# Kernel tuning notes

Measured on AMD Instinct MI355X. Metric: run time of the kernel, lower is better.

Reference implementation:

```python
import jax, jax.numpy as jnp
import numpy as np

B, S, H, E, TOPK = 8, 512, 1024, 8, 2


def setup_inputs() -> dict:
    key = jax.random.key(0)
    ks = jax.random.split(key, 10)
    D = 2 * H
    inp = {
        "vector": jax.random.normal(ks[0], (B, S, D), dtype=jnp.float32),
        # gate weights (Linear(H, E)): stored as [H, E] for x @ W + b
        "Wg": jax.random.normal(ks[1], (H, E), dtype=jnp.float32) * 0.02,
        "bg": jnp.zeros((E,), dtype=jnp.float32),
        "Wf": jax.random.normal(ks[2], (H, E), dtype=jnp.float32) * 0.02,
        "bf": jnp.zeros((E,), dtype=jnp.float32),
        # expert MLP weights, stacked over experts: Linear(2H,2H) -> ReLU -> Linear(2H,2H)
        "W1": jax.random.normal(ks[3], (E, D, D), dtype=jnp.float32) * 0.02,
        "b1": jnp.zeros((E, D), dtype=jnp.float32),
        "W2": jax.random.normal(ks[4], (E, D, D), dtype=jnp.float32) * 0.02,
        "b2": jnp.zeros((E, D), dtype=jnp.float32),
        # combine weights (config['initializer_weight'])
        "weight": jnp.ones((2,), dtype=jnp.float32),
        "top_k": TOPK,
    }
    return inp


def reference(vector, Wg, bg, Wf, bf, W1, b1, W2, b2, weight, top_k):
    h = Wg.shape[0]
    n_exp = Wg.shape[1]
    # gate_g on first half, softmax, then top-k sparsify (scatter of topk values)
    rout_g = jax.nn.softmax(vector[:, :, :h] @ Wg + bg, axis=-1)           # [B,S,E]
    vals, idx = jax.lax.top_k(rout_g, top_k)                               # [B,S,k]
    route_g = jnp.sum(jax.nn.one_hot(idx, n_exp, dtype=vals.dtype) * vals[..., None], axis=-2)  # [B,S,E]
    # gate_f on second half: dense softmax routing
    rout_f = jax.nn.softmax(vector[:, :, h:2 * h] @ Wf + bf, axis=-1)      # [B,S,E]
    # dense expert computation for every token (dropout = identity at eval)
    hidden = jax.nn.relu(jnp.einsum('bsd,edh->bseh', vector, W1) + b1)     # [B,S,E,2H]
    expert_out = jnp.einsum('bseh,ehd->bsed', hidden, W2) + b2             # [B,S,E,2H]
    out0 = weight[0] * jnp.einsum('bsed,bse->bsd', expert_out[..., :h], route_g)
    out1 = weight[1] * jnp.einsum('bsed,bse->bsd', expert_out[..., h:2 * h], rout_f)
    return (out0, out1)
```

## Files before the change

### kernel.cpp

```cpp
#include <hip/hip_runtime.h>

#define TOKENS 4096
#define DDIM   2048
#define HDIM   1024
#define NEXP   8
#define GK     2048
#define GN     2048

typedef __bf16 bf16_t;
typedef __bf16 bf16x8 __attribute__((ext_vector_type(8)));
typedef __bf16 bf16x4 __attribute__((ext_vector_type(4)));
typedef float  f32x4  __attribute__((ext_vector_type(4)));

__device__ inline void gld_lds16(const bf16_t* g, bf16_t* l) {
  __builtin_amdgcn_global_load_lds(
      (const __attribute__((address_space(1))) void*)g,
      (__attribute__((address_space(3))) void*)l, 16, 0, 0);
}

__global__ __launch_bounds__(256)
void k_routing(const float* __restrict__ vec,
               const float* __restrict__ Wg, const float* __restrict__ bg,
               const float* __restrict__ Wf, const float* __restrict__ bfv,
               const float* __restrict__ wgt,
               float* __restrict__ c0, float* __restrict__ c1)
{
  const int wave = threadIdx.x >> 6;
  const int lane = threadIdx.x & 63;
  const int m = blockIdx.x * 4 + wave;
  const float* v = vec + (size_t)m * DDIM;

  float ag[NEXP], af[NEXP];
#pragma unroll
  for (int e = 0; e < NEXP; ++e) { ag[e] = 0.f; af[e] = 0.f; }

  for (int i = lane; i < HDIM; i += 64) {
    const float xg = v[i];
    const float xf = v[HDIM + i];
    const float4 wg0 = *(const float4*)(Wg + i * NEXP);
    const float4 wg1 = *(const float4*)(Wg + i * NEXP + 4);
    const float4 wf0 = *(const float4*)(Wf + i * NEXP);
    const float4 wf1 = *(const float4*)(Wf + i * NEXP + 4);
    ag[0] += xg * wg0.x; ag[1] += xg * wg0.y; ag[2] += xg * wg0.z; ag[3] += xg * wg0.w;
    ag[4] += xg * wg1.x; ag[5] += xg * wg1.y; ag[6] += xg * wg1.z; ag[7] += xg * wg1.w;
    af[0] += xf * wf0.x; af[1] += xf * wf0.y; af[2] += xf * wf0.z; af[3] += xf * wf0.w;
    af[4] += xf * wf1.x; af[5] += xf * wf1.y; af[6] += xf * wf1.z; af[7] += xf * wf1.w;
  }
#pragma unroll
  for (int e = 0; e < NEXP; ++e) {
#pragma unroll
    for (int off = 32; off >= 1; off >>= 1) {
      ag[e] += __shfl_xor(ag[e], off, 64);
      af[e] += __shfl_xor(af[e], off, 64);
    }
  }
  if (lane == 0) {
    float g[NEXP], f[NEXP];
    float mg = -1e30f, mf = -1e30f;
#pragma unroll
    for (int e = 0; e < NEXP; ++e) {
      g[e] = ag[e] + bg[e]; mg = fmaxf(mg, g[e]);
      f[e] = af[e] + bfv[e]; mf = fmaxf(mf, f[e]);
    }
    float sg = 0.f, sf = 0.f;
#pragma unroll
    for (int e = 0; e < NEXP; ++e) {
      g[e] = expf(g[e] - mg); sg += g[e];
      f[e] = expf(f[e] - mf); sf += f[e];
    }
    const float rg = 1.f / sg, rf = 1.f / sf;
#pragma unroll
    for (int e = 0; e < NEXP; ++e) { g[e] *= rg; f[e] *= rf; }
    int i1 = 0;
#pragma unroll
    for (int e = 1; e < NEXP; ++e) if (g[e] > g[i1]) i1 = e;
    int i2 = (i1 == 0) ? 1 : 0;
#pragma unroll
    for (int e = 0; e < NEXP; ++e) if (e != i1 && g[e] > g[i2]) i2 = e;
    const float w0 = wgt[0], w1 = wgt[1];
#pragma unroll
    for (int e = 0; e < NEXP; ++e) {
      c0[e * TOKENS + m] = (e == i1 || e == i2) ? w0 * g[e] : 0.f;
      c1[e * TOKENS + m] = w1 * f[e];
    }
  }
}

__global__ __launch_bounds__(256)
void k_cvt(const float* __restrict__ in, bf16_t* __restrict__ out)
{
  const size_t i = ((size_t)blockIdx.x * 256 + threadIdx.x) * 8;
  const float4 a = *(const float4*)(in + i);
  const float4 b = *(const float4*)(in + i + 4);
  bf16x8 o;
  o[0] = (bf16_t)a.x; o[1] = (bf16_t)a.y; o[2] = (bf16_t)a.z; o[3] = (bf16_t)a.w;
  o[4] = (bf16_t)b.x; o[5] = (bf16_t)b.y; o[6] = (bf16_t)b.z; o[7] = (bf16_t)b.w;
  *(bf16x8*)(out + i) = o;
}

#define TP 68
__global__ __launch_bounds__(256)
void k_cvt_wt(const float* __restrict__ W, bf16_t* __restrict__ Wt)
{
  __shared__ __attribute__((aligned(16))) bf16_t tile[64 * TP];
  const size_t eoff = (size_t)blockIdx.z * DDIM * DDIM;
  const float* w = W + eoff;
  bf16_t* wt = Wt + eoff;
  const int k0 = blockIdx.x * 64;
  const int n0 = blockIdx.y * 64;
  const int t = threadIdx.x;
  const int c4 = (t & 15) * 4;
  const int rb = (t >> 4) * 4;
#pragma unroll
  for (int rr = 0; rr < 4; ++rr) {
    const int r = rb + rr;
    const float4 v = *(const float4*)(w + (size_t)(k0 + r) * DDIM + n0 + c4);
    tile[(c4 + 0) * TP + r] = (bf16_t)v.x;
    tile[(c4 + 1) * TP + r] = (bf16_t)v.y;
    tile[(c4 + 2) * TP + r] = (bf16_t)v.z;
    tile[(c4 + 3) * TP + r] = (bf16_t)v.w;
  }
  __syncthreads();
  const int nl = t >> 2;
  const int kq = (t & 3) * 16;
  bf16_t* dst = wt + (size_t)(n0 + nl) * DDIM + k0 + kq;
#pragma unroll
  for (int j2 = 0; j2 < 4; ++j2) {
    bf16x4 u = *(const bf16x4*)(&tile[nl * TP + kq + j2 * 4]);
    *(bf16x4*)(dst + j2 * 4) = u;
  }
}

__global__ __launch_bounds__(256, 2)
void k_gemm_relu(const bf16_t* __restrict__ A, const bf16_t* __restrict__ W1t,
                 const float* __restrict__ b1, bf16_t* __restrict__ Hd)
{
  __shared__ __attribute__((aligned(16))) bf16_t As[128 * 32];
  __shared__ __attribute__((aligned(16))) bf16_t Bs[128 * 32];
  const int e = blockIdx.z;
  const bf16_t* Bt = W1t + (size_t)e * GK * GN;
  const float* bias = b1 + (size_t)e * GN;
  bf16_t* H = Hd + (size_t)e * TOKENS * GN;

  const int t = threadIdx.x;
  const int wave = t >> 6;
  const int lane = t & 63;
  const int m0 = blockIdx.x * 128;
  const int n0 = blockIdx.y * 128;
  const int wm = (wave >> 1) << 6;
  const int wn = (wave & 1) << 6;

  f32x4 acc[4][4] = {};

  const bf16_t* aP0 = A + (size_t)(m0 + (t >> 2)) * GK + (t & 3) * 8;
  const bf16_t* aP1 = aP0 + (size_t)64 * GK;
  const bf16_t* bP0 = Bt + (size_t)(n0 + (t >> 2)) * GK + (t & 3) * 8;
  const bf16_t* bP1 = bP0 + (size_t)64 * GK;
  bf16_t* lA0 = As + wave * 512;
  bf16_t* lA1 = As + 2048 + wave * 512;
  bf16_t* lB0 = Bs + wave * 512;
  bf16_t* lB1 = Bs + 2048 + wave * 512;

  const int fr = lane & 15;
  const int kq = (lane >> 4) * 8;

  for (int k0 = 0; k0 < GK; k0 += 32) {
    gld_lds16(aP0 + k0, lA0);
    gld_lds16(aP1 + k0, lA1);
    gld_lds16(bP0 + k0, lB0);
    gld_lds16(bP1 + k0, lB1);
    __syncthreads();
    bf16x8 afr[4], bfr[4];
#pragma unroll
    for (int i = 0; i < 4; ++i) {
      afr[i] = *(const bf16x8*)(As + (wm + i * 16 + fr) * 32 + kq);
      bfr[i] = *(const bf16x8*)(Bs + (wn + i * 16 + fr) * 32 + kq);
    }
#pragma unroll
    for (int i = 0; i < 4; ++i)
#pragma unroll
      for (int j = 0; j < 4; ++j)
        acc[i][j] = __builtin_amdgcn_mfma_f32_16x16x32_bf16(afr[i], bfr[j], acc[i][j], 0, 0, 0);
    __syncthreads();
  }

  const int col = lane & 15;
  const int rq  = (lane >> 4) * 4;
#pragma unroll
  for (int j = 0; j < 4; ++j) {
    const int gn = n0 + wn + j * 16 + col;
    const float bv = bias[gn];
#pragma unroll
    for (int i = 0; i < 4; ++i) {
      const int gm = m0 + wm + i * 16 + rq;
#pragma unroll
      for (int r = 0; r < 4; ++r) {
        float v = acc[i][j][r] + bv;
        v = v > 0.f ? v : 0.f;
        H[(size_t)(gm + r) * GN + gn] = (bf16_t)v;
      }
    }
  }
}

__global__ __launch_bounds__(256, 2)
void k_gemm2_sum(const bf16_t* __restrict__ Hd, const bf16_t* __restrict__ W2t,
                 const float* __restrict__ b2,
                 const float* __restrict__ c0, const float* __restrict__ c1,
                 float* __restrict__ out0, float* __restrict__ out1)
{
  __shared__ __attribute__((aligned(16))) bf16_t As[128 * 32];
  __shared__ __attribute__((aligned(16))) bf16_t Bs[128 * 32];
  __shared__ float cs[NEXP][128];
  __shared__ float bs[NEXP][128];

  const int t = threadIdx.x;
  const int wave = t >> 6;
  const int lane = t & 63;
  const int m0 = blockIdx.x * 128;
  const int n0 = blockIdx.y * 128;
  const int wm = (wave >> 1) << 6;
  const int wn = (wave & 1) << 6;

  const bool hi = (n0 >= HDIM);
  const float* cc = hi ? c1 : c0;

#pragma unroll
  for (int idx = t; idx < NEXP * 128; idx += 256) {
    const int e = idx >> 7, r = idx & 127;
    cs[e][r] = cc[e * TOKENS + m0 + r];
    bs[e][r] = b2[e * DDIM + n0 + r];
  }

  f32x4 fin[4][4] = {};

  const int fr = lane & 15;
  const int kq = (lane >> 4) * 8;
  const int rowOff = (t >> 2);
  const int kOff = (t & 3) * 8;
  bf16_t* lA0 = As + wave * 512;
  bf16_t* lA1 = As + 2048 + wave * 512;
  bf16_t* lB0 = Bs + wave * 512;
  bf16_t* lB1 = Bs + 2048 + wave * 512;

  for (int e = 0; e < NEXP; ++e) {
    const bf16_t* aP0 = Hd + (size_t)e * TOKENS * GK + (size_t)(m0 + rowOff) * GK + kOff;
    const bf16_t* aP1 = aP0 + (size_t)64 * GK;
    const bf16_t* bP0 = W2t + (size_t)e * GN * GK + (size_t)(n0 + rowOff) * GK + kOff;
    const bf16_t* bP1 = bP0 + (size_t)64 * GK;

    f32x4 acc[4][4] = {};
    for (int k0 = 0; k0 < GK; k0 += 32) {
      gld_lds16(aP0 + k0, lA0);
      gld_lds16(aP1 + k0, lA1);
      gld_lds16(bP0 + k0, lB0);
      gld_lds16(bP1 + k0, lB1);
      __syncthreads();
      bf16x8 afr[4], bfr[4];
#pragma unroll
      for (int i = 0; i < 4; ++i) {
        afr[i] = *(const bf16x8*)(As + (wm + i * 16 + fr) * 32 + kq);
        bfr[i] = *(const bf16x8*)(Bs + (wn + i * 16 + fr) * 32 + kq);
      }
#pragma unroll
      for (int i = 0; i < 4; ++i)
#pragma unroll
        for (int j = 0; j < 4; ++j)
          acc[i][j] = __builtin_amdgcn_mfma_f32_16x16x32_bf16(afr[i], bfr[j], acc[i][j], 0, 0, 0);
      __syncthreads();
    }

    const int colL = wn + (lane & 15);
    const int rqL  = wm + (lane >> 4) * 4;
#pragma unroll
    for (int j = 0; j < 4; ++j) {
      const float bv = bs[e][colL + j * 16];
#pragma unroll
      for (int i = 0; i < 4; ++i) {
#pragma unroll
        for (int r = 0; r < 4; ++r) {
          const float ce = cs[e][rqL + i * 16 + r];
          fin[i][j][r] += ce * (acc[i][j][r] + bv);
        }
      }
    }
  }

  const int col = lane & 15;
  const int rq  = (lane >> 4) * 4;
#pragma unroll
  for (int j = 0; j < 4; ++j) {
    const int gn = n0 + wn + j * 16 + col;
    float* obase = hi ? (out1 + (gn - HDIM)) : (out0 + gn);
#pragma unroll
    for (int i = 0; i < 4; ++i) {
      const int gm = m0 + wm + i * 16 + rq;
#pragma unroll
      for (int r = 0; r < 4; ++r)
        obase[(size_t)(gm + r) * HDIM] = fin[i][j][r];
    }
  }
}

__global__ __launch_bounds__(256, 2)
void k_gemm_out(const bf16_t* __restrict__ A, const bf16_t* __restrict__ Bt,
                const float* __restrict__ bias,
                const float* __restrict__ c0, const float* __restrict__ c1,
                float* __restrict__ out0, float* __restrict__ out1, const int accum)
{
  __shared__ __attribute__((aligned(16))) bf16_t As[128 * 32];
  __shared__ __attribute__((aligned(16))) bf16_t Bs[128 * 32];
  const int t = threadIdx.x;
  const int wave = t >> 6;
  const int lane = t & 63;
  const int m0 = blockIdx.x * 128;
  const int n0 = blockIdx.y * 128;
  const int wm = (wave >> 1) << 6;
  const int wn = (wave & 1) << 6;

  f32x4 acc[4][4] = {};

  const bf16_t* aP0 = A + (size_t)(m0 + (t >> 2)) * GK + (t & 3) * 8;
  const bf16_t* aP1 = aP0 + (size_t)64 * GK;
  const bf16_t* bP0 = Bt + (size_t)(n0 + (t >> 2)) * GK + (t & 3) * 8;
  const bf16_t* bP1 = bP0 + (size_t)64 * GK;
  bf16_t* lA0 = As + wave * 512;
  bf16_t* lA1 = As + 2048 + wave * 512;
  bf16_t* lB0 = Bs + wave * 512;
  bf16_t* lB1 = Bs + 2048 + wave * 512;

  const int fr = lane & 15;
  const int kq = (lane >> 4) * 8;

  for (int k0 = 0; k0 < GK; k0 += 32) {
    gld_lds16(aP0 + k0, lA0);
    gld_lds16(aP1 + k0, lA1);
    gld_lds16(bP0 + k0, lB0);
    gld_lds16(bP1 + k0, lB1);
    __syncthreads();
    bf16x8 afr[4], bfr[4];
#pragma unroll
    for (int i = 0; i < 4; ++i) {
      afr[i] = *(const bf16x8*)(As + (wm + i * 16 + fr) * 32 + kq);
      bfr[i] = *(const bf16x8*)(Bs + (wn + i * 16 + fr) * 32 + kq);
    }
#pragma unroll
    for (int i = 0; i < 4; ++i)
#pragma unroll
      for (int j = 0; j < 4; ++j)
        acc[i][j] = __builtin_amdgcn_mfma_f32_16x16x32_bf16(afr[i], bfr[j], acc[i][j], 0, 0, 0);
    __syncthreads();
  }

  const int col = lane & 15;
  const int rq  = (lane >> 4) * 4;
#pragma unroll
  for (int j = 0; j < 4; ++j) {
    const int gn = n0 + wn + j * 16 + col;
    const float bv = bias[gn];
    const bool lo = gn < HDIM;
    float* obase = lo ? (out0 + gn) : (out1 + (gn - HDIM));
    const float* cc = lo ? c0 : c1;
#pragma unroll
    for (int i = 0; i < 4; ++i) {
      const int gmB = m0 + wm + i * 16 + rq;
#pragma unroll
      for (int r = 0; r < 4; ++r) {
        const int gm = gmB + r;
        float v = (acc[i][j][r] + bv) * cc[gm];
        float* dst = obase + (size_t)gm * HDIM;
        if (accum) v += *dst;
        *dst = v;
      }
    }
  }
}

extern "C" void kernel_launch(void* const* d_in, const int* in_sizes, int n_in,
                              void* d_out, int out_size, void* d_ws, size_t ws_size,
                              hipStream_t stream)
{
  const float* vec = (const float*)d_in[0];
  const float* Wg  = (const float*)d_in[1];
  const float* bg  = (const float*)d_in[2];
  const float* Wf  = (const float*)d_in[3];
  const float* bfv = (const float*)d_in[4];
  const float* W1  = (const float*)d_in[5];
  const float* b1  = (const float*)d_in[6];
  const float* W2  = (const float*)d_in[7];
  const float* b2  = (const float*)d_in[8];
  const float* wgt = (const float*)d_in[9];

  float* out0 = (float*)d_out;
  float* out1 = out0 + (size_t)TOKENS * HDIM;

  char* base = (char*)d_ws;
  const size_t XB = (size_t)TOKENS * DDIM * 2;
  const size_t HB = (size_t)NEXP * TOKENS * DDIM * 2;
  const size_t WT = (size_t)NEXP * DDIM * DDIM * 2;

  bf16_t* Xbf = (bf16_t*)base;
  float*  c0  = (float*)(base + XB);
  float*  c1  = c0 + (size_t)NEXP * TOKENS;
  size_t off = XB + 2 * (size_t)NEXP * TOKENS * 4;

  k_routing<<<dim3(TOKENS / 4), 256, 0, stream>>>(vec, Wg, bg, Wf, bfv, wgt, c0, c1);
  k_cvt<<<dim3((TOKENS * DDIM) / 2048), 256, 0, stream>>>(vec, Xbf);

  if (ws_size >= off + HB + 2 * WT) {
    bf16_t* hidden = (bf16_t*)(base + off);
    bf16_t* W1t    = (bf16_t*)(base + off + HB);
    bf16_t* W2t    = (bf16_t*)(base + off + HB + WT);
    k_cvt_wt<<<dim3(32, 32, NEXP), 256, 0, stream>>>(W1, W1t);
    k_cvt_wt<<<dim3(32, 32, NEXP), 256, 0, stream>>>(W2, W2t);
    k_gemm_relu<<<dim3(32, 16, NEXP), 256, 0, stream>>>(Xbf, W1t, b1, hidden);
    k_gemm2_sum<<<dim3(32, 16), 256, 0, stream>>>(hidden, W2t, b2, c0, c1, out0, out1);
  } else {
    bf16_t* hidden = (bf16_t*)(base + off);
    bf16_t* W1t    = hidden + (size_t)TOKENS * DDIM;
    bf16_t* W2t    = W1t + (size_t)DDIM * DDIM;
    for (int e = 0; e < NEXP; ++e) {
      k_cvt_wt<<<dim3(32, 32, 1), 256, 0, stream>>>(W1 + (size_t)e * DDIM * DDIM, W1t);
      k_cvt_wt<<<dim3(32, 32, 1), 256, 0, stream>>>(W2 + (size_t)e * DDIM * DDIM, W2t);
      k_gemm_relu<<<dim3(32, 16, 1), 256, 0, stream>>>(Xbf, W1t, b1 + (size_t)e * DDIM, hidden);
      k_gemm_out<<<dim3(32, 16), 256, 0, stream>>>(
          hidden, W2t, b2 + (size_t)e * DDIM,
          c0 + (size_t)e * TOKENS, c1 + (size_t)e * TOKENS, out0, out1, e > 0);
    }
  }
}
```

Before: 1.072 ms.

## Rewrite both expert GEMMs with 8-wave 256x128 tiles and 4-stage LDS pipeline

Replaces the 4-wave 128x128 expert GEMM kernels with 512-thread kernels. Each block computes a 256x128 tile, and the two GEMMs run as k_gemm1_8p and k_gemm2_8p. Global-to-LDS loads go through a four-buffer ring issued three stages ahead, so loads overlap the MFMA work. The kernels also use an XOR-swizzled LDS layout, explicit vmcnt/lgkmcnt waits with raw barriers, and s_setprio around the MFMA bursts. In exchange, the LDS footprint per block grows, which may limit resident blocks, and the second GEMM's grid shrinks to 256 blocks.

```diff
diff --git a/kernel.cpp b/kernel.cpp
--- a/kernel.cpp
+++ b/kernel.cpp
@@ -17,6 +17,10 @@
       (const __attribute__((address_space(1))) void*)g,
       (__attribute__((address_space(3))) void*)l, 16, 0, 0);
 }
+
+#define LGKM0() asm volatile("s_waitcnt lgkmcnt(0)" ::: "memory")
+#define VMC(n)  asm volatile("s_waitcnt vmcnt(" #n ")" ::: "memory")
+#define BAR()   __builtin_amdgcn_s_barrier()
 
 __global__ __launch_bounds__(256)
 void k_routing(const float* __restrict__ vec,
@@ -131,6 +135,188 @@
   }
 }
 
+
+#define FRG(base, R, KQ) \
+  (*(const bf16x8*)((base) + ((((R) * 32 + (KQ)) ^ ((((R) >> 3) & 1) << 4)))))
+
+#define MFMA_(d, x, y) (d) = __builtin_amdgcn_mfma_f32_16x16x32_bf16((x), (y), (d), 0, 0, 0)
+
+#define PHASE(U, PA, STA, STB, NP) do { \
+    bf16x8 _a[8], _b0, _b1; \
+    _Pragma("unroll") \
+    for (int _i = 0; _i < 8; ++_i) _a[_i] = FRG(AsF + (U) * 8192, wm + _i * 16 + fr, kq); \
+    _b0 = FRG(BsF + (U) * 4096, wn + fr, kq); \
+    _b1 = FRG(BsF + (U) * 4096, wn + 16 + fr, kq); \
+    if ((PA) < (NP)) { STA(PA, (PA) & 3); STB(PA, (PA) & 3); } \
+    BAR(); LGKM0(); \
+    __builtin_amdgcn_s_setprio(1); \
+    _Pragma("unroll") \
+    for (int _i = 0; _i < 8; ++_i) { MFMA_(acc[_i][0], _a[_i], _b0); MFMA_(acc[_i][1], _a[_i], _b1); } \
+    __builtin_amdgcn_s_setprio(0); \
+  } while (0)
+
+#define TILE(U0, U1, PA, PB, STA, STB, NP) do { \
+    PHASE(U0, PA, STA, STB, NP); \
+    BAR(); \
+    PHASE(U1, PB, STA, STB, NP); \
+    if ((PB) < (NP)) { VMC(3); } else { VMC(0); } \
+    BAR(); \
+  } while (0)
+
+__global__ __launch_bounds__(512, 2)
+void k_gemm1_8p(const bf16_t* __restrict__ A, const bf16_t* __restrict__ W1t,
+                const float* __restrict__ b1, bf16_t* __restrict__ Hd)
+{
+  __shared__ __attribute__((aligned(16))) bf16_t AsF[4 * 8192];
+  __shared__ __attribute__((aligned(16))) bf16_t BsF[4 * 4096];
+  const int e = blockIdx.z;
+  const int t = threadIdx.x;
+  const int wave = t >> 6, lane = t & 63;
+  const int m0 = blockIdx.x * 256, n0 = blockIdx.y * 128;
+  const int wm = (wave >> 2) * 128, wn = (wave & 3) * 32;
+  const int fr = lane & 15, kq = (lane >> 4) * 8;
+
+  const int sRw = wave * 16 + (lane >> 2);
+  const int sC  = ((lane & 3) * 8) ^ (((lane >> 5) & 1) << 4);
+  const bf16_t* aSrc = A + (size_t)(m0 + sRw) * GK + sC;
+  const bf16_t* bSrc = W1t + (size_t)e * GN * GK + (size_t)(n0 + sRw) * GK + sC;
+  bf16_t* aDst = AsF + wave * 512;
+  bf16_t* bDst = BsF + wave * 512;
+
+#define STA1(p, u) do { const bf16_t* _s = aSrc + (size_t)(p) * 32; \
+    gld_lds16(_s, aDst + (u) * 8192); \
+    gld_lds16(_s + (size_t)128 * GK, aDst + (u) * 8192 + 4096); } while (0)
+#define STB1(p, u) gld_lds16(bSrc + (size_t)(p) * 32, bDst + (u) * 4096)
+
+  f32x4 acc[8][2] = {};
+
+  STA1(0, 0); STB1(0, 0);
+  STA1(1, 1); STB1(1, 1);
+  STA1(2, 2); STB1(2, 2);
+  asm volatile("s_waitcnt vmcnt(3)" ::: "memory");
+  BAR();
+
+#pragma unroll 1
+  for (int tt = 0; tt < 32; tt += 2) {
+    TILE(0, 1, 2 * tt + 3, 2 * tt + 4, STA1, STB1, 64);
+    TILE(2, 3, 2 * tt + 5, 2 * tt + 6, STA1, STB1, 64);
+  }
+
+  const float* bias = b1 + (size_t)e * DDIM;
+  bf16_t* Hb = Hd + (size_t)e * TOKENS * DDIM;
+  const int ecol = lane & 15, erow = (lane >> 4) * 4;
+#pragma unroll
+  for (int j = 0; j < 2; ++j) {
+    const int gn = n0 + wn + j * 16 + ecol;
+    const float bv = bias[gn];
+#pragma unroll
+    for (int i = 0; i < 8; ++i) {
+      const int gm = m0 + wm + i * 16 + erow;
+#pragma unroll
+      for (int r = 0; r < 4; ++r) {
+        float v = acc[i][j][r] + bv;
+        v = v > 0.f ? v : 0.f;
+        Hb[(size_t)(gm + r) * DDIM + gn] = (bf16_t)v;
+      }
+    }
+  }
+#undef STA1
+#undef STB1
+}
+
+__global__ __launch_bounds__(512, 2)
+void k_gemm2_8p(const bf16_t* __restrict__ Hd, const bf16_t* __restrict__ W2t,
+                const float* __restrict__ b2,
+                const float* __restrict__ c0, const float* __restrict__ c1,
+                float* __restrict__ out0, float* __restrict__ out1)
+{
+  __shared__ __attribute__((aligned(16))) bf16_t AsF[4 * 8192];
+  __shared__ __attribute__((aligned(16))) bf16_t BsF[4 * 4096];
+  __shared__ float cs[NEXP][256];
+  __shared__ float bsh[NEXP][128];
+
+  const int t = threadIdx.x;
+  const int wave = t >> 6, lane = t & 63;
+  const int m0 = blockIdx.x * 256, n0 = blockIdx.y * 128;
+  const int wm = (wave >> 2) * 128, wn = (wave & 3) * 32;
+  const int fr = lane & 15, kq = (lane >> 4) * 8;
+  const bool hi = (n0 >= HDIM);
+  const float* cc = hi ? c1 : c0;
+
+  for (int idx = t; idx < NEXP * 256; idx += 512) {
+    const int ee = idx >> 8, r = idx & 255;
+    cs[ee][r] = cc[ee * TOKENS + m0 + r];
+  }
+  for (int idx = t; idx < NEXP * 128; idx += 512) {
+    const int ee = idx >> 7, r = idx & 127;
+    bsh[ee][r] = b2[ee * DDIM + n0 + r];
+  }
+
+  const int sRw = wave * 16 + (lane >> 2);
+  const int sC  = ((lane & 3) * 8) ^ (((lane >> 5) & 1) << 4);
+  const bf16_t* aSrc = Hd + (size_t)(m0 + sRw) * GK + sC;
+  const bf16_t* bSrc = W2t + (size_t)(n0 + sRw) * GK + sC;
+  bf16_t* aDst = AsF + wave * 512;
+  bf16_t* bDst = BsF + wave * 512;
+
+#define STA2(p, u) do { \
+    const bf16_t* _s = aSrc + (size_t)((p) >> 6) * ((size_t)TOKENS * GK) + (size_t)(((p) & 63) * 32); \
+    gld_lds16(_s, aDst + (u) * 8192); \
+    gld_lds16(_s + (size_t)128 * GK, aDst + (u) * 8192 + 4096); } while (0)
+#define STB2(p, u) do { \
+    const bf16_t* _s = bSrc + (size_t)((p) >> 6) * ((size_t)GN * GK) + (size_t)(((p) & 63) * 32); \
+    gld_lds16(_s, bDst + (u) * 4096); } while (0)
+
+  f32x4 acc[8][2] = {};
+  f32x4 fin[8][2] = {};
+
+  STA2(0, 0); STB2(0, 0);
+  STA2(1, 1); STB2(1, 1);
+  STA2(2, 2); STB2(2, 2);
+  asm volatile("s_waitcnt vmcnt(3) lgkmcnt(0)" ::: "memory");
+  BAR();
+
+  const int ecol = lane & 15, erow = (lane >> 4) * 4;
+
+#pragma unroll 1
+  for (int ex = 0; ex < NEXP; ++ex) {
+#pragma unroll 1
+    for (int tt = 0; tt < 32; tt += 2) {
+      const int gt = ex * 32 + tt;
+      TILE(0, 1, 2 * gt + 3, 2 * gt + 4, STA2, STB2, 512);
+      TILE(2, 3, 2 * gt + 5, 2 * gt + 6, STA2, STB2, 512);
+    }
+#pragma unroll
+    for (int j = 0; j < 2; ++j) {
+      const float bv = bsh[ex][wn + j * 16 + ecol];
+#pragma unroll
+      for (int i = 0; i < 8; ++i) {
+        const int rw = wm + i * 16 + erow;
+#pragma unroll
+        for (int r = 0; r < 4; ++r) {
+          fin[i][j][r] += cs[ex][rw + r] * (acc[i][j][r] + bv);
+          acc[i][j][r] = 0.f;
+        }
+      }
+    }
+  }
+
+#pragma unroll
+  for (int j = 0; j < 2; ++j) {
+    const int gn = n0 + wn + j * 16 + ecol;
+    float* ob = hi ? (out1 + (gn - HDIM)) : (out0 + gn);
+#pragma unroll
+    for (int i = 0; i < 8; ++i) {
+      const int gm = m0 + wm + i * 16 + erow;
+#pragma unroll
+      for (int r = 0; r < 4; ++r)
+        ob[(size_t)(gm + r) * HDIM] = fin[i][j][r];
+    }
+  }
+#undef STA2
+#undef STB2
+}
+
 __global__ __launch_bounds__(256, 2)
 void k_gemm_relu(const bf16_t* __restrict__ A, const bf16_t* __restrict__ W1t,
                  const float* __restrict__ b1, bf16_t* __restrict__ Hd)
@@ -199,105 +385,6 @@
         v = v > 0.f ? v : 0.f;
         H[(size_t)(gm + r) * GN + gn] = (bf16_t)v;
       }
-    }
-  }
-}
-
-__global__ __launch_bounds__(256, 2)
-void k_gemm2_sum(const bf16_t* __restrict__ Hd, const bf16_t* __restrict__ W2t,
-                 const float* __restrict__ b2,
-                 const float* __restrict__ c0, const float* __restrict__ c1,
-                 float* __restrict__ out0, float* __restrict__ out1)
-{
-  __shared__ __attribute__((aligned(16))) bf16_t As[128 * 32];
-  __shared__ __attribute__((aligned(16))) bf16_t Bs[128 * 32];
-  __shared__ float cs[NEXP][128];
-  __shared__ float bs[NEXP][128];
-
-  const int t = threadIdx.x;
-  const int wave = t >> 6;
-  const int lane = t & 63;
-  const int m0 = blockIdx.x * 128;
-  const int n0 = blockIdx.y * 128;
-  const int wm = (wave >> 1) << 6;
-  const int wn = (wave & 1) << 6;
-
-  const bool hi = (n0 >= HDIM);
-  const float* cc = hi ? c1 : c0;
-
-#pragma unroll
-  for (int idx = t; idx < NEXP * 128; idx += 256) {
-    const int e = idx >> 7, r = idx & 127;
-    cs[e][r] = cc[e * TOKENS + m0 + r];
-    bs[e][r] = b2[e * DDIM + n0 + r];
-  }
-
-  f32x4 fin[4][4] = {};
-
-  const int fr = lane & 15;
-  const int kq = (lane >> 4) * 8;
-  const int rowOff = (t >> 2);
-  const int kOff = (t & 3) * 8;
-  bf16_t* lA0 = As + wave * 512;
-  bf16_t* lA1 = As + 2048 + wave * 512;
-  bf16_t* lB0 = Bs + wave * 512;
-  bf16_t* lB1 = Bs + 2048 + wave * 512;
-
-  for (int e = 0; e < NEXP; ++e) {
-    const bf16_t* aP0 = Hd + (size_t)e * TOKENS * GK + (size_t)(m0 + rowOff) * GK + kOff;
-    const bf16_t* aP1 = aP0 + (size_t)64 * GK;
-    const bf16_t* bP0 = W2t + (size_t)e * GN * GK + (size_t)(n0 + rowOff) * GK + kOff;
-    const bf16_t* bP1 = bP0 + (size_t)64 * GK;
-
-    f32x4 acc[4][4] = {};
-    for (int k0 = 0; k0 < GK; k0 += 32) {
-      gld_lds16(aP0 + k0, lA0);
-      gld_lds16(aP1 + k0, lA1);
-      gld_lds16(bP0 + k0, lB0);
-      gld_lds16(bP1 + k0, lB1);
-      __syncthreads();
-      bf16x8 afr[4], bfr[4];
-#pragma unroll
-      for (int i = 0; i < 4; ++i) {
-        afr[i] = *(const bf16x8*)(As + (wm + i * 16 + fr) * 32 + kq);
-        bfr[i] = *(const bf16x8*)(Bs + (wn + i * 16 + fr) * 32 + kq);
-      }
-#pragma unroll
-      for (int i = 0; i < 4; ++i)
-#pragma unroll
-        for (int j = 0; j < 4; ++j)
-          acc[i][j] = __builtin_amdgcn_mfma_f32_16x16x32_bf16(afr[i], bfr[j], acc[i][j], 0, 0, 0);
-      __syncthreads();
-    }
-
-    const int colL = wn + (lane & 15);
-    const int rqL  = wm + (lane >> 4) * 4;
-#pragma unroll
-    for (int j = 0; j < 4; ++j) {
-      const float bv = bs[e][colL + j * 16];
-#pragma unroll
-      for (int i = 0; i < 4; ++i) {
-#pragma unroll
-        for (int r = 0; r < 4; ++r) {
-          const float ce = cs[e][rqL + i * 16 + r];
-          fin[i][j][r] += ce * (acc[i][j][r] + bv);
-        }
-      }
-    }
-  }
-
-  const int col = lane & 15;
-  const int rq  = (lane >> 4) * 4;
-#pragma unroll
-  for (int j = 0; j < 4; ++j) {
-    const int gn = n0 + wn + j * 16 + col;
-    float* obase = hi ? (out1 + (gn - HDIM)) : (out0 + gn);
-#pragma unroll
-    for (int i = 0; i < 4; ++i) {
-      const int gm = m0 + wm + i * 16 + rq;
-#pragma unroll
-      for (int r = 0; r < 4; ++r)
-        obase[(size_t)(gm + r) * HDIM] = fin[i][j][r];
     }
   }
 }
@@ -413,8 +500,8 @@
     bf16_t* W2t    = (bf16_t*)(base + off + HB + WT);
     k_cvt_wt<<<dim3(32, 32, NEXP), 256, 0, stream>>>(W1, W1t);
     k_cvt_wt<<<dim3(32, 32, NEXP), 256, 0, stream>>>(W2, W2t);
-    k_gemm_relu<<<dim3(32, 16, NEXP), 256, 0, stream>>>(Xbf, W1t, b1, hidden);
-    k_gemm2_sum<<<dim3(32, 16), 256, 0, stream>>>(hidden, W2t, b2, c0, c1, out0, out1);
+    k_gemm1_8p<<<dim3(16, 16, NEXP), 512, 0, stream>>>(Xbf, W1t, b1, hidden);
+    k_gemm2_8p<<<dim3(16, 16), 512, 0, stream>>>(hidden, W2t, b2, c0, c1, out0, out1);
   } else {
     bf16_t* hidden = (bf16_t*)(base + off);
     bf16_t* W1t    = hidden + (size_t)TOKENS * DDIM;
```

Result: faster. 1.049 ms (-2.1%).
